# Kernel tuning notes

Measured on AMD Instinct MI355X. Metric: run time of the kernel, lower is better.

## Reference

```python
import jax, jax.numpy as jnp
import numpy as np

ALPHA = 1.5
A = 0.5
BANDWIDTH = 1.0
SPHERE_RADIUS = 1.0
HIDDEN = 1024
HEAD = 64
EPS_ACOS = 1e-07
EPS_NORM = 1e-12  # torch F.normalize clamp_min eps


def _l2norm(v):
    # F.normalize(v, p=2, dim=-1)
    n = jnp.sqrt(jnp.sum(v * v, axis=-1, keepdims=True))
    return v / jnp.maximum(n, EPS_NORM)


def setup_inputs() -> dict:
    key = jax.random.key(0)
    ks = jax.random.split(key, 7)
    B, S = 8, 2048
    s = 1.0 / np.sqrt(HIDDEN)
    return {
        "x": jax.random.normal(ks[0], (B, S, HIDDEN), dtype=jnp.float32),
        "Wq": jax.random.uniform(ks[1], (HIDDEN, HEAD), jnp.float32, -s, s),
        "bq": jax.random.uniform(ks[2], (HEAD,), jnp.float32, -s, s),
        "Wk": jax.random.uniform(ks[3], (HIDDEN, HEAD), jnp.float32, -s, s),
        "bk": jax.random.uniform(ks[4], (HEAD,), jnp.float32, -s, s),
        "Wv": jax.random.uniform(ks[5], (HIDDEN, HEAD), jnp.float32, -s, s),
        "bv": jax.random.uniform(ks[6], (HEAD,), jnp.float32, -s, s),
    }


def reference(x, Wq, bq, Wk, bk, Wv, bv):
    # q,k,v: [B,S,HEAD], L2-normalized along feature axis
    q = _l2norm(jnp.einsum("bsh,hd->bsd", x, Wq) + bq)
    k = _l2norm(jnp.einsum("bsh,hd->bsd", x, Wk) + bk)
    v = _l2norm(jnp.einsum("bsh,hd->bsd", x, Wv) + bv)

    # geodesic distance on sphere: [B,S,S]
    cos = jnp.einsum("bqd,bkd->bqk", q, k)
    g_dist = jnp.arccos(jnp.clip(cos, -1.0 + EPS_ACOS, 1.0 - EPS_ACOS)) * SPHERE_RADIUS

    # alpha < 2 -> power-law score
    score = (1.0 + g_dist / jnp.sqrt(BANDWIDTH)) ** (-HEAD - ALPHA)

    # dual degree normalization (a != 0): diag(row^-a) @ S @ diag(col^-a),
    # expressed as broadcast row/col scaling (same math, no diag_embed matmuls)
    r = jnp.sum(score, axis=-1) ** (-A)  # [B,Sq]
    c = jnp.sum(score, axis=-2) ** (-A)  # [B,Sk]
    k_tilde = r[..., :, None] * score * c[..., None, :]

    # L1 normalize over key axis (F.normalize p=1): entries are positive
    denom = jnp.maximum(jnp.sum(jnp.abs(k_tilde), axis=-1, keepdims=True), EPS_NORM)
    probs = k_tilde / denom

    out = jnp.einsum("bqk,bkd->bqd", probs, v)
    return (out, probs)
```

## Files before the change

kernel.cpp:

```cpp
#include <hip/hip_runtime.h>
#include <math.h>

#define BB 8
#define SS 2048
#define HH 1024
#define DD 64
#define NCV 65

typedef __attribute__((ext_vector_type(8))) short bf16x8;
typedef __attribute__((ext_vector_type(4))) float f32x4;
typedef __attribute__((ext_vector_type(16))) float f32x16;

#define MFMA16(a, b, c) __builtin_amdgcn_mfma_f32_16x16x32_bf16(a, b, c, 0, 0, 0)
#define MFMA32(a, b, c) __builtin_amdgcn_mfma_f32_32x32x16_bf16(a, b, c, 0, 0, 0)

__device__ __forceinline__ ushort bf16rne(float f) {
    uint u = __float_as_uint(f);
    uint r = (u + 0x7FFFu + ((u >> 16) & 1u)) >> 16;
    return (ushort)r;
}
__device__ __forceinline__ float bf2f(ushort h) {
    return __uint_as_float(((uint)h) << 16);
}

__device__ __forceinline__ float score_fn(float cosv) {
    float ax = fminf(fabsf(cosv), 1.0f - 1e-7f);
    float p = fmaf(ax, -0.0012624911f, 0.0066700901f);
    p = fmaf(ax, p, -0.0170881256f);
    p = fmaf(ax, p, 0.0308918810f);
    p = fmaf(ax, p, -0.0501743046f);
    p = fmaf(ax, p, 0.0889789874f);
    p = fmaf(ax, p, -0.2145988016f);
    p = fmaf(ax, p, 1.5707963050f);
    float r = sqrtf(1.0f - ax) * p;
    float g = (cosv >= 0.0f) ? r : (3.14159265358979f - r);
    return exp2f(-65.5f * log2f(1.0f + g));
}

__global__ __launch_bounds__(256) void k_prep(
    const float* __restrict__ Wq, const float* __restrict__ Wk, const float* __restrict__ Wv,
    const float* __restrict__ bq, const float* __restrict__ bk, const float* __restrict__ bv,
    ushort* __restrict__ Whi, ushort* __restrict__ Wlo, float* __restrict__ bcat)
{
    const int n = blockIdx.x;
    const int m = n >> 6, d = n & 63;
    const float* W = (m == 0) ? Wq : (m == 1 ? Wk : Wv);
    #pragma unroll
    for (int i = 0; i < 4; ++i) {
        int j = i * 256 + threadIdx.x;
        float f = W[(size_t)j * DD + d];
        ushort h = bf16rne(f);
        Whi[(size_t)n * HH + j] = h;
        Wlo[(size_t)n * HH + j] = bf16rne(f - bf2f(h));
    }
    if (n == 0 && threadIdx.x < 192) {
        int t = threadIdx.x, mm = t >> 6, dd = t & 63;
        const float* b = (mm == 0) ? bq : (mm == 1 ? bk : bv);
        bcat[t] = b[dd];
    }
}

__global__ __launch_bounds__(256) void k_projmm(
    const float* __restrict__ x, const ushort* __restrict__ Whi,
    const ushort* __restrict__ Wlo, const float* __restrict__ bcat,
    ushort* __restrict__ qh, ushort* __restrict__ ql,
    ushort* __restrict__ kh, ushort* __restrict__ kl,
    float* __restrict__ vw)
{
    __shared__ __align__(16) char smem[32 * 193 * 4];
    __shared__ float rns[96];
    __shared__ float bsh[192];
    ushort* xhi = (ushort*)smem;
    ushort* xlo = xhi + 32 * 128;
    float* ctile = (float*)smem;

    const int t = threadIdx.x;
    const int lane = t & 63;
    const int wid = t >> 6;
    const int row0 = blockIdx.x * 32;
    if (t < 192) bsh[t] = bcat[t];

    f32x4 acc[2][3];
    #pragma unroll
    for (int ar = 0; ar < 2; ++ar)
        #pragma unroll
        for (int bc = 0; bc < 3; ++bc)
            acc[ar][bc] = (f32x4){0.f, 0.f, 0.f, 0.f};

    for (int ch = 0; ch < 8; ++ch) {
        const int j0 = ch * 128;
        __syncthreads();
        #pragma unroll
        for (int i = 0; i < 2; ++i) {
            int u = i * 256 + t;
            int row = u >> 4, uc = u & 15;
            const float* xp = &x[(size_t)(row0 + row) * HH + j0 + uc * 8];
            float4 a = *(const float4*)xp;
            float4 b = *(const float4*)(xp + 4);
            float fs[8] = {a.x, a.y, a.z, a.w, b.x, b.y, b.z, b.w};
            bf16x8 hv, lv;
            #pragma unroll
            for (int e = 0; e < 8; ++e) {
                ushort h = bf16rne(fs[e]);
                hv[e] = (short)h;
                lv[e] = (short)bf16rne(fs[e] - bf2f(h));
            }
            int su = uc ^ (row & 7);
            *(bf16x8*)(xhi + row * 128 + su * 8) = hv;
            *(bf16x8*)(xlo + row * 128 + su * 8) = lv;
        }
        __syncthreads();
        #pragma unroll
        for (int ks = 0; ks < 4; ++ks) {
            bf16x8 ah[2], al[2], bh[3], bl[3];
            #pragma unroll
            for (int ar = 0; ar < 2; ++ar) {
                int row = ar * 16 + (lane & 15);
                int su = (ks * 4 + (lane >> 4)) ^ (row & 7);
                ah[ar] = *(const bf16x8*)(xhi + row * 128 + su * 8);
                al[ar] = *(const bf16x8*)(xlo + row * 128 + su * 8);
            }
            const int koff = j0 + ks * 32 + (lane >> 4) * 8;
            #pragma unroll
            for (int bc = 0; bc < 3; ++bc) {
                int n = wid * 48 + bc * 16 + (lane & 15);
                bh[bc] = *(const bf16x8*)(Whi + (size_t)n * HH + koff);
                bl[bc] = *(const bf16x8*)(Wlo + (size_t)n * HH + koff);
            }
            #pragma unroll
            for (int ar = 0; ar < 2; ++ar)
                #pragma unroll
                for (int bc = 0; bc < 3; ++bc) {
                    acc[ar][bc] = MFMA16(ah[ar], bh[bc], acc[ar][bc]);
                    acc[ar][bc] = MFMA16(ah[ar], bl[bc], acc[ar][bc]);
                    acc[ar][bc] = MFMA16(al[ar], bh[bc], acc[ar][bc]);
                }
        }
    }
    __syncthreads();
    #pragma unroll
    for (int ar = 0; ar < 2; ++ar)
        #pragma unroll
        for (int bc = 0; bc < 3; ++bc) {
            int n = wid * 48 + bc * 16 + (lane & 15);
            #pragma unroll
            for (int r = 0; r < 4; ++r) {
                int row = ar * 16 + (lane >> 4) * 4 + r;
                ctile[row * 193 + n] = acc[ar][bc][r];
            }
        }
    __syncthreads();
    if (t < 96) {
        int mat = t >> 5, row = t & 31;
        float ss = 0.f;
        #pragma unroll 8
        for (int d = 0; d < 64; ++d) {
            float v = ctile[row * 193 + mat * 64 + d] + bsh[mat * 64 + d];
            ss = fmaf(v, v, ss);
        }
        rns[t] = 1.0f / fmaxf(sqrtf(ss), 1e-12f);
    }
    __syncthreads();
    #pragma unroll
    for (int i = 0; i < 24; ++i) {
        int idx = i * 256 + t;
        int row = idx / 192;
        int n = idx - row * 192;
        float v = (ctile[row * 193 + n] + bsh[n]) * rns[(n >> 6) * 32 + row];
        size_t off = (size_t)(row0 + row) * DD + (n & 63);
        if (n < 64) {
            ushort h = bf16rne(v);
            qh[off] = h; ql[off] = bf16rne(v - bf2f(h));
        } else if (n < 128) {
            ushort h = bf16rne(v);
            kh[off] = h; kl[off] = bf16rne(v - bf2f(h));
        } else {
            vw[off] = v;
        }
    }
}

#define K_LOAD(H0,H1,H2,H3,L0,L1,L2,L3, KT) { \
    const ushort* kp = kh + (size_t)(b * SS + kbase + (KT) * 32 + qrow) * DD + kg; \
    const ushort* lp = kl + (size_t)(b * SS + kbase + (KT) * 32 + qrow) * DD + kg; \
    H0 = *(const bf16x8*)(kp);      L0 = *(const bf16x8*)(lp); \
    H1 = *(const bf16x8*)(kp + 16); L1 = *(const bf16x8*)(lp + 16); \
    H2 = *(const bf16x8*)(kp + 32); L2 = *(const bf16x8*)(lp + 32); \
    H3 = *(const bf16x8*)(kp + 48); L3 = *(const bf16x8*)(lp + 48); }

#define K_COMPUTE(H0,H1,H2,H3,L0,L1,L2,L3, KT) { \
    f32x16 acc = Z16; \
    acc = MFMA32(H0, qbh0, acc); acc = MFMA32(H0, qbl0, acc); acc = MFMA32(L0, qbh0, acc); \
    acc = MFMA32(H1, qbh1, acc); acc = MFMA32(H1, qbl1, acc); acc = MFMA32(L1, qbh1, acc); \
    acc = MFMA32(H2, qbh2, acc); acc = MFMA32(H2, qbl2, acc); acc = MFMA32(L2, qbh2, acc); \
    acc = MFMA32(H3, qbh3, acc); acc = MFMA32(H3, qbl3, acc); acc = MFMA32(L3, qbh3, acc); \
    const int kloc = kbase + (KT) * 32 + hi4; \
    uint2 wv; \
    wv.x = (uint)bf16rne(score_fn(acc[0]))  | ((uint)bf16rne(score_fn(acc[1]))  << 16); \
    wv.y = (uint)bf16rne(score_fn(acc[2]))  | ((uint)bf16rne(score_fn(acc[3]))  << 16); \
    *(uint2*)(srow + kloc) = wv; \
    wv.x = (uint)bf16rne(score_fn(acc[4]))  | ((uint)bf16rne(score_fn(acc[5]))  << 16); \
    wv.y = (uint)bf16rne(score_fn(acc[6]))  | ((uint)bf16rne(score_fn(acc[7]))  << 16); \
    *(uint2*)(srow + kloc + 8) = wv; \
    wv.x = (uint)bf16rne(score_fn(acc[8]))  | ((uint)bf16rne(score_fn(acc[9]))  << 16); \
    wv.y = (uint)bf16rne(score_fn(acc[10])) | ((uint)bf16rne(score_fn(acc[11])) << 16); \
    *(uint2*)(srow + kloc + 16) = wv; \
    wv.x = (uint)bf16rne(score_fn(acc[12])) | ((uint)bf16rne(score_fn(acc[13])) << 16); \
    wv.y = (uint)bf16rne(score_fn(acc[14])) | ((uint)bf16rne(score_fn(acc[15])) << 16); \
    *(uint2*)(srow + kloc + 24) = wv; }

__global__ __launch_bounds__(256, 4) void k_score(
    const ushort* __restrict__ qh, const ushort* __restrict__ ql,
    const ushort* __restrict__ kh, const ushort* __restrict__ kl,
    ushort* __restrict__ scrS)
{
    const int t = threadIdx.x;
    const int lane = t & 63;
    const int w = t >> 6;
    const int bid = blockIdx.x;
    const int b  = bid >> 8;
    const int q0 = ((bid >> 2) & 63) * 32;
    const int kbase = (bid & 3) * 512 + w * 128;
    const int qrow = lane & 31;
    const int kg = (lane >> 5) * 8;
    const int hi4 = (lane >> 5) * 4;
    const f32x16 Z16 = {0.f,0.f,0.f,0.f,0.f,0.f,0.f,0.f,0.f,0.f,0.f,0.f,0.f,0.f,0.f,0.f};

    const size_t qoff = (size_t)(b * SS + q0 + qrow) * DD + kg;
    bf16x8 qbh0 = *(const bf16x8*)(qh + qoff);
    bf16x8 qbh1 = *(const bf16x8*)(qh + qoff + 16);
    bf16x8 qbh2 = *(const bf16x8*)(qh + qoff + 32);
    bf16x8 qbh3 = *(const bf16x8*)(qh + qoff + 48);
    bf16x8 qbl0 = *(const bf16x8*)(ql + qoff);
    bf16x8 qbl1 = *(const bf16x8*)(ql + qoff + 16);
    bf16x8 qbl2 = *(const bf16x8*)(ql + qoff + 32);
    bf16x8 qbl3 = *(const bf16x8*)(ql + qoff + 48);
    ushort* srow = scrS + (size_t)(b * SS + q0 + qrow) * 4096 + 2048;

    bf16x8 xh0, xh1, xh2, xh3, xl0, xl1, xl2, xl3;
    bf16x8 yh0, yh1, yh2, yh3, yl0, yl1, yl2, yl3;
    K_LOAD(xh0,xh1,xh2,xh3,xl0,xl1,xl2,xl3, 0)
    K_LOAD(yh0,yh1,yh2,yh3,yl0,yl1,yl2,yl3, 1)
    K_COMPUTE(xh0,xh1,xh2,xh3,xl0,xl1,xl2,xl3, 0)
    K_LOAD(xh0,xh1,xh2,xh3,xl0,xl1,xl2,xl3, 2)
    K_COMPUTE(yh0,yh1,yh2,yh3,yl0,yl1,yl2,yl3, 1)
    K_LOAD(yh0,yh1,yh2,yh3,yl0,yl1,yl2,yl3, 3)
    K_COMPUTE(xh0,xh1,xh2,xh3,xl0,xl1,xl2,xl3, 2)
    K_COMPUTE(yh0,yh1,yh2,yh3,yl0,yl1,yl2,yl3, 3)
}

__global__ __launch_bounds__(256) void k_csum(
    const ushort* __restrict__ scrS, float* __restrict__ colsum)
{
    __shared__ float cls[32][64];
    const int t = threadIdx.x;
    const int bid = blockIdx.x;
    const int b  = bid >> 8;
    const int k0 = ((bid >> 3) & 31) * 64;
    const int qs = (bid & 7) * 256;
    const int tq = t >> 3, tk = t & 7;
    float colacc[8];
    #pragma unroll
    for (int e = 0; e < 8; ++e) colacc[e] = 0.f;
    #pragma unroll 2
    for (int it = 0; it < 8; ++it) {
        int q = qs + it * 32 + tq;
        bf16x8 s8 = *(const bf16x8*)(scrS + (size_t)(b * SS + q) * 4096 + 2048 + k0 + tk * 8);
        #pragma unroll
        for (int e = 0; e < 8; ++e) colacc[e] += bf2f((ushort)s8[e]);
    }
    #pragma unroll
    for (int e = 0; e < 8; ++e) cls[tq][tk * 8 + e] = colacc[e];
    __syncthreads();
    if (t < 64) {
        float s = 0.f;
        #pragma unroll
        for (int i = 0; i < 32; ++i) s += cls[i][t];
        atomicAdd(&colsum[b * SS + k0 + t], s);
    }
}

__global__ __launch_bounds__(256) void k_cvc(
    const float* __restrict__ vw, const float* __restrict__ colsum,
    ushort* __restrict__ cvT)
{
    __shared__ float vs[128][68];
    const int t = threadIdx.x;
    const int b = blockIdx.x >> 4;
    const int k0 = (blockIdx.x & 15) * 128;
    #pragma unroll
    for (int i = 0; i < 8; ++i) {
        int idx = i * 256 + t;
        int r = idx >> 4, c4 = idx & 15;
        float4 v4 = *(const float4*)&vw[(size_t)(b * SS + k0 + r) * DD + c4 * 4];
        *(float4*)&vs[r][c4 * 4] = v4;
    }
    __syncthreads();
    const int tk = t & 127;
    const int tj = t >> 7;
    float c = 1.0f / sqrtf(colsum[b * SS + k0 + tk]);
    #pragma unroll
    for (int jj = 0; jj < 32; ++jj) {
        int j = jj * 2 + tj;
        cvT[((size_t)b * NCV + j) * SS + k0 + tk] = bf16rne(c * vs[tk][j]);
    }
    if (tj == 0) cvT[((size_t)b * NCV + 64) * SS + k0 + tk] = bf16rne(c);
}

__global__ __launch_bounds__(256, 4) void k_nd(
    const ushort* __restrict__ scrS, const ushort* __restrict__ cvT,
    float* __restrict__ dinv_g, float* __restrict__ out)
{
    __shared__ float nred[16][64];
    __shared__ float dPart[4][16];
    __shared__ float dInv[16];
    const int t = threadIdx.x;
    const int lane = t & 63;
    const int w = t >> 6;
    const int b = blockIdx.x >> 7;
    const int q0 = (blockIdx.x & 127) * 16;
    const int kbase = w * 512;
    const int qn = lane & 15;
    const int g = lane >> 4;

    ((float*)nred)[t] = 0.f; ((float*)nred)[t + 256] = 0.f;
    ((float*)nred)[t + 512] = 0.f; ((float*)nred)[t + 768] = 0.f;
    __syncthreads();

    const ushort* cslice = cvT + (size_t)b * NCV * SS;
    const ushort* cbrow = cslice + (size_t)64 * SS;
    const ushort* srow = scrS + (size_t)(b * SS + q0 + qn) * 4096 + 2048;

    float dacc = 0.f;
    f32x4 nacc[4];
    #pragma unroll
    for (int ct = 0; ct < 4; ++ct) nacc[ct] = (f32x4){0.f, 0.f, 0.f, 0.f};

    #pragma unroll 4
    for (int ch = 0; ch < 16; ++ch) {
        const int ks0 = kbase + ch * 32;
        bf16x8 s8 = *(const bf16x8*)(srow + ks0 + g * 8);
        bf16x8 c8 = *(const bf16x8*)(cbrow + ks0 + g * 8);
        #pragma unroll
        for (int e = 0; e < 8; ++e)
            dacc = fmaf(bf2f((ushort)s8[e]), bf2f((ushort)c8[e]), dacc);
        #pragma unroll
        for (int ct = 0; ct < 4; ++ct) {
            bf16x8 bfv = *(const bf16x8*)(cslice + (size_t)(ct * 16 + qn) * SS + ks0 + g * 8);
            nacc[ct] = MFMA16(s8, bfv, nacc[ct]);
        }
    }
    {
        float d = dacc;
        d += __shfl_xor(d, 16, 64);
        d += __shfl_xor(d, 32, 64);
        if (lane < 16) dPart[w][lane] = d;
    }
    __syncthreads();
    if (t < 16) {
        float di = 1.0f / (dPart[0][t] + dPart[1][t] + dPart[2][t] + dPart[3][t]);
        dInv[t] = di;
        dinv_g[b * SS + q0 + t] = di;
    }
    #pragma unroll
    for (int ct = 0; ct < 4; ++ct)
        #pragma unroll
        for (int r = 0; r < 4; ++r)
            atomicAdd(&nred[g * 4 + r][ct * 16 + qn], nacc[ct][r]);
    __syncthreads();
    {
        int q = t >> 4, c4 = (t & 15) * 4;
        float di = dInv[q];
        float4 o;
        o.x = nred[q][c4] * di;     o.y = nred[q][c4 + 1] * di;
        o.z = nred[q][c4 + 2] * di; o.w = nred[q][c4 + 3] * di;
        *(float4*)&out[(size_t)(b * SS + q0 + q) * DD + c4] = o;
    }
}

__global__ __launch_bounds__(256) void k_probs(
    const ushort* __restrict__ scrS, const ushort* __restrict__ cvT,
    const float* __restrict__ dinv_g, float* __restrict__ probs)
{
    const int t = threadIdx.x;
    const int b = blockIdx.x >> 8;
    const int r0 = (blockIdx.x & 255) * 8;
    const ushort* cbrow = cvT + ((size_t)b * NCV + 64) * SS;

    float cf[8];
    {
        bf16x8 c8 = *(const bf16x8*)(cbrow + t * 8);
        #pragma unroll
        for (int e = 0; e < 8; ++e) cf[e] = bf2f((ushort)c8[e]);
    }
    bf16x8 s8[8];
    float di[8];
    #pragma unroll
    for (int r = 0; r < 8; ++r) {
        s8[r] = *(const bf16x8*)(scrS + (size_t)(b * SS + r0 + r) * 4096 + 2048 + t * 8);
        di[r] = dinv_g[b * SS + r0 + r];
    }
    __syncthreads();
    #pragma unroll
    for (int r = 0; r < 8; ++r) {
        float4 o0, o1;
        o0.x = bf2f((ushort)s8[r][0]) * cf[0] * di[r];
        o0.y = bf2f((ushort)s8[r][1]) * cf[1] * di[r];
        o0.z = bf2f((ushort)s8[r][2]) * cf[2] * di[r];
        o0.w = bf2f((ushort)s8[r][3]) * cf[3] * di[r];
        o1.x = bf2f((ushort)s8[r][4]) * cf[4] * di[r];
        o1.y = bf2f((ushort)s8[r][5]) * cf[5] * di[r];
        o1.z = bf2f((ushort)s8[r][6]) * cf[6] * di[r];
        o1.w = bf2f((ushort)s8[r][7]) * cf[7] * di[r];
        float* prow = probs + (size_t)(b * SS + r0 + r) * SS + t * 8;
        *(float4*)prow = o0;
        *(float4*)(prow + 4) = o1;
    }
}

extern "C" void kernel_launch(void* const* d_in, const int* in_sizes, int n_in,
                              void* d_out, int out_size, void* d_ws, size_t ws_size,
                              hipStream_t stream)
{
    const float* x  = (const float*)d_in[0];
    const float* Wq = (const float*)d_in[1];
    const float* bq = (const float*)d_in[2];
    const float* Wk = (const float*)d_in[3];
    const float* bk = (const float*)d_in[4];
    const float* Wv = (const float*)d_in[5];
    const float* bv = (const float*)d_in[6];

    float* out   = (float*)d_out;
    float* probs = out + (size_t)BB * SS * DD;
    ushort* scrS = (ushort*)probs;

    const size_t NQ = (size_t)BB * SS * DD;
    ushort* qh    = (ushort*)d_ws;
    ushort* ql    = qh + NQ;
    ushort* kh    = ql + NQ;
    ushort* kl    = kh + NQ;
    float*  vw    = (float*)(kl + NQ);
    float*  colsum = vw + NQ;
    float*  dinv  = colsum + BB * SS;
    ushort* cvT   = (ushort*)(dinv + BB * SS);
    ushort* Whi   = cvT + (size_t)BB * NCV * SS;
    ushort* Wlo   = Whi + (size_t)192 * HH;
    float*  bcat  = (float*)(Wlo + (size_t)192 * HH);

    hipMemsetAsync(colsum, 0, BB * SS * sizeof(float), stream);
    k_prep  <<<192, 256, 0, stream>>>(Wq, Wk, Wv, bq, bk, bv, Whi, Wlo, bcat);
    k_projmm<<<512, 256, 0, stream>>>(x, Whi, Wlo, bcat, qh, ql, kh, kl, vw);
    k_score <<<2048, 256, 0, stream>>>(qh, ql, kh, kl, scrS);
    k_csum  <<<2048, 256, 0, stream>>>(scrS, colsum);
    k_cvc   <<<128, 256, 0, stream>>>(vw, colsum, cvT);
    k_nd    <<<1024, 256, 0, stream>>>(scrS, cvT, dinv, out);
    k_probs <<<2048, 256, 0, stream>>>(scrS, cvT, dinv, probs);
}
```

Measured before the change: 227.4 us.

## Fuse normalization and probs write into one kernel; coalesce cvT writes

Merges the denominator/output kernel with the probs-writing kernel, so each block computes its row inverse degree in shared memory and then writes its own probs rows. This removes the global dinv buffer and one kernel launch, and the second read of the score rows is more likely to hit cache. The k_cvc transpose now works on 64-column tiles and writes packed 4-element chunks so stores are coalesced. Also switches to the library bf16 conversion, uses pointer-increment addressing in the MFMA loop, and writes probs with nontemporal stores. The in-place aliasing of scores inside the probs buffer stays correct only because each block reads its own rows before the barrier that precedes overwriting them.

```diff
diff --git a/kernel.cpp b/kernel.cpp
--- a/kernel.cpp
+++ b/kernel.cpp
@@ -1,4 +1,5 @@
 #include <hip/hip_runtime.h>
+#include <hip/hip_bf16.h>
 #include <math.h>
 
 #define BB 8
@@ -18,6 +19,10 @@
     uint u = __float_as_uint(f);
     uint r = (u + 0x7FFFu + ((u >> 16) & 1u)) >> 16;
     return (ushort)r;
+}
+__device__ __forceinline__ ushort bfc(float f) {
+    __hip_bfloat16 h = __float2bfloat16(f);
+    return *reinterpret_cast<ushort*>(&h);
 }
 __device__ __forceinline__ float bf2f(ushort h) {
     return __uint_as_float(((uint)h) << 16);
@@ -196,17 +201,17 @@
     acc = MFMA32(H3, qbh3, acc); acc = MFMA32(H3, qbl3, acc); acc = MFMA32(L3, qbh3, acc); \
     const int kloc = kbase + (KT) * 32 + hi4; \
     uint2 wv; \
-    wv.x = (uint)bf16rne(score_fn(acc[0]))  | ((uint)bf16rne(score_fn(acc[1]))  << 16); \
-    wv.y = (uint)bf16rne(score_fn(acc[2]))  | ((uint)bf16rne(score_fn(acc[3]))  << 16); \
+    wv.x = (uint)bfc(score_fn(acc[0]))  | ((uint)bfc(score_fn(acc[1]))  << 16); \
+    wv.y = (uint)bfc(score_fn(acc[2]))  | ((uint)bfc(score_fn(acc[3]))  << 16); \
     *(uint2*)(srow + kloc) = wv; \
-    wv.x = (uint)bf16rne(score_fn(acc[4]))  | ((uint)bf16rne(score_fn(acc[5]))  << 16); \
-    wv.y = (uint)bf16rne(score_fn(acc[6]))  | ((uint)bf16rne(score_fn(acc[7]))  << 16); \
+    wv.x = (uint)bfc(score_fn(acc[4]))  | ((uint)bfc(score_fn(acc[5]))  << 16); \
+    wv.y = (uint)bfc(score_fn(acc[6]))  | ((uint)bfc(score_fn(acc[7]))  << 16); \
     *(uint2*)(srow + kloc + 8) = wv; \
-    wv.x = (uint)bf16rne(score_fn(acc[8]))  | ((uint)bf16rne(score_fn(acc[9]))  << 16); \
-    wv.y = (uint)bf16rne(score_fn(acc[10])) | ((uint)bf16rne(score_fn(acc[11])) << 16); \
+    wv.x = (uint)bfc(score_fn(acc[8]))  | ((uint)bfc(score_fn(acc[9]))  << 16); \
+    wv.y = (uint)bfc(score_fn(acc[10])) | ((uint)bfc(score_fn(acc[11])) << 16); \
     *(uint2*)(srow + kloc + 16) = wv; \
-    wv.x = (uint)bf16rne(score_fn(acc[12])) | ((uint)bf16rne(score_fn(acc[13])) << 16); \
-    wv.y = (uint)bf16rne(score_fn(acc[14])) | ((uint)bf16rne(score_fn(acc[15])) << 16); \
+    wv.x = (uint)bfc(score_fn(acc[12])) | ((uint)bfc(score_fn(acc[13])) << 16); \
+    wv.y = (uint)bfc(score_fn(acc[14])) | ((uint)bfc(score_fn(acc[15])) << 16); \
     *(uint2*)(srow + kloc + 24) = wv; }
 
 __global__ __launch_bounds__(256, 4) void k_score(
@@ -284,32 +289,42 @@
     const float* __restrict__ vw, const float* __restrict__ colsum,
     ushort* __restrict__ cvT)
 {
-    __shared__ float vs[128][68];
+    __shared__ float vs[64][65];
+    __shared__ float csh[64];
     const int t = threadIdx.x;
-    const int b = blockIdx.x >> 4;
-    const int k0 = (blockIdx.x & 15) * 128;
-    #pragma unroll
-    for (int i = 0; i < 8; ++i) {
+    const int b = blockIdx.x >> 5;
+    const int k0 = (blockIdx.x & 31) * 64;
+    #pragma unroll
+    for (int i = 0; i < 4; ++i) {
         int idx = i * 256 + t;
         int r = idx >> 4, c4 = idx & 15;
         float4 v4 = *(const float4*)&vw[(size_t)(b * SS + k0 + r) * DD + c4 * 4];
         *(float4*)&vs[r][c4 * 4] = v4;
     }
-    __syncthreads();
-    const int tk = t & 127;
-    const int tj = t >> 7;
-    float c = 1.0f / sqrtf(colsum[b * SS + k0 + tk]);
-    #pragma unroll
-    for (int jj = 0; jj < 32; ++jj) {
-        int j = jj * 2 + tj;
-        cvT[((size_t)b * NCV + j) * SS + k0 + tk] = bf16rne(c * vs[tk][j]);
-    }
-    if (tj == 0) cvT[((size_t)b * NCV + 64) * SS + k0 + tk] = bf16rne(c);
-}
-
-__global__ __launch_bounds__(256, 4) void k_nd(
+    if (t < 64) csh[t] = 1.0f / sqrtf(colsum[b * SS + k0 + t]);
+    __syncthreads();
+    const int kk4 = (t & 15) * 4;
+    #pragma unroll
+    for (int jt = 0; jt < 4; ++jt) {
+        int j = jt * 16 + (t >> 4);
+        uint2 wv;
+        wv.x = (uint)bfc(csh[kk4 + 0] * vs[kk4 + 0][j])
+             | ((uint)bfc(csh[kk4 + 1] * vs[kk4 + 1][j]) << 16);
+        wv.y = (uint)bfc(csh[kk4 + 2] * vs[kk4 + 2][j])
+             | ((uint)bfc(csh[kk4 + 3] * vs[kk4 + 3][j]) << 16);
+        *(uint2*)(cvT + ((size_t)b * NCV + j) * SS + k0 + kk4) = wv;
+    }
+    if (t < 16) {
+        uint2 wv;
+        wv.x = (uint)bfc(csh[t * 4 + 0]) | ((uint)bfc(csh[t * 4 + 1]) << 16);
+        wv.y = (uint)bfc(csh[t * 4 + 2]) | ((uint)bfc(csh[t * 4 + 3]) << 16);
+        *(uint2*)(cvT + ((size_t)b * NCV + 64) * SS + k0 + t * 4) = wv;
+    }
+}
+
+__global__ __launch_bounds__(256, 4) void k_ndp(
     const ushort* __restrict__ scrS, const ushort* __restrict__ cvT,
-    float* __restrict__ dinv_g, float* __restrict__ out)
+    float* __restrict__ probs, float* __restrict__ out)
 {
     __shared__ float nred[16][64];
     __shared__ float dPart[4][16];
@@ -329,26 +344,35 @@
 
     const ushort* cslice = cvT + (size_t)b * NCV * SS;
     const ushort* cbrow = cslice + (size_t)64 * SS;
-    const ushort* srow = scrS + (size_t)(b * SS + q0 + qn) * 4096 + 2048;
 
     float dacc = 0.f;
     f32x4 nacc[4];
     #pragma unroll
     for (int ct = 0; ct < 4; ++ct) nacc[ct] = (f32x4){0.f, 0.f, 0.f, 0.f};
 
+    const ushort* sp = scrS + (size_t)(b * SS + q0 + qn) * 4096 + 2048 + kbase + g * 8;
+    const ushort* cp = cbrow + kbase + g * 8;
+    const ushort* p0 = cslice + (size_t)(0 * 16 + qn) * SS + kbase + g * 8;
+    const ushort* p1 = cslice + (size_t)(1 * 16 + qn) * SS + kbase + g * 8;
+    const ushort* p2 = cslice + (size_t)(2 * 16 + qn) * SS + kbase + g * 8;
+    const ushort* p3 = cslice + (size_t)(3 * 16 + qn) * SS + kbase + g * 8;
+
     #pragma unroll 4
     for (int ch = 0; ch < 16; ++ch) {
-        const int ks0 = kbase + ch * 32;
-        bf16x8 s8 = *(const bf16x8*)(srow + ks0 + g * 8);
-        bf16x8 c8 = *(const bf16x8*)(cbrow + ks0 + g * 8);
+        bf16x8 s8 = *(const bf16x8*)sp;
+        bf16x8 c8 = *(const bf16x8*)cp;
+        bf16x8 b0 = *(const bf16x8*)p0;
+        bf16x8 b1 = *(const bf16x8*)p1;
+        bf16x8 b2 = *(const bf16x8*)p2;
+        bf16x8 b3 = *(const bf16x8*)p3;
         #pragma unroll
         for (int e = 0; e < 8; ++e)
             dacc = fmaf(bf2f((ushort)s8[e]), bf2f((ushort)c8[e]), dacc);
-        #pragma unroll
-        for (int ct = 0; ct < 4; ++ct) {
-            bf16x8 bfv = *(const bf16x8*)(cslice + (size_t)(ct * 16 + qn) * SS + ks0 + g * 8);
-            nacc[ct] = MFMA16(s8, bfv, nacc[ct]);
-        }
+        nacc[0] = MFMA16(s8, b0, nacc[0]);
+        nacc[1] = MFMA16(s8, b1, nacc[1]);
+        nacc[2] = MFMA16(s8, b2, nacc[2]);
+        nacc[3] = MFMA16(s8, b3, nacc[3]);
+        sp += 32; cp += 32; p0 += 32; p1 += 32; p2 += 32; p3 += 32;
     }
     {
         float d = dacc;
@@ -357,11 +381,7 @@
         if (lane < 16) dPart[w][lane] = d;
     }
     __syncthreads();
-    if (t < 16) {
-        float di = 1.0f / (dPart[0][t] + dPart[1][t] + dPart[2][t] + dPart[3][t]);
-        dInv[t] = di;
-        dinv_g[b * SS + q0 + t] = di;
-    }
+    if (t < 16) dInv[t] = 1.0f / (dPart[0][t] + dPart[1][t] + dPart[2][t] + dPart[3][t]);
     #pragma unroll
     for (int ct = 0; ct < 4; ++ct)
         #pragma unroll
@@ -376,45 +396,38 @@
         o.z = nred[q][c4 + 2] * di; o.w = nred[q][c4 + 3] * di;
         *(float4*)&out[(size_t)(b * SS + q0 + q) * DD + c4] = o;
     }
-}
-
-__global__ __launch_bounds__(256) void k_probs(
-    const ushort* __restrict__ scrS, const ushort* __restrict__ cvT,
-    const float* __restrict__ dinv_g, float* __restrict__ probs)
-{
-    const int t = threadIdx.x;
-    const int b = blockIdx.x >> 8;
-    const int r0 = (blockIdx.x & 255) * 8;
-    const ushort* cbrow = cvT + ((size_t)b * NCV + 64) * SS;
-
     float cf[8];
     {
         bf16x8 c8 = *(const bf16x8*)(cbrow + t * 8);
         #pragma unroll
         for (int e = 0; e < 8; ++e) cf[e] = bf2f((ushort)c8[e]);
     }
-    bf16x8 s8[8];
-    float di[8];
-    #pragma unroll
-    for (int r = 0; r < 8; ++r) {
-        s8[r] = *(const bf16x8*)(scrS + (size_t)(b * SS + r0 + r) * 4096 + 2048 + t * 8);
-        di[r] = dinv_g[b * SS + r0 + r];
-    }
-    __syncthreads();
-    #pragma unroll
-    for (int r = 0; r < 8; ++r) {
-        float4 o0, o1;
-        o0.x = bf2f((ushort)s8[r][0]) * cf[0] * di[r];
-        o0.y = bf2f((ushort)s8[r][1]) * cf[1] * di[r];
-        o0.z = bf2f((ushort)s8[r][2]) * cf[2] * di[r];
-        o0.w = bf2f((ushort)s8[r][3]) * cf[3] * di[r];
-        o1.x = bf2f((ushort)s8[r][4]) * cf[4] * di[r];
-        o1.y = bf2f((ushort)s8[r][5]) * cf[5] * di[r];
-        o1.z = bf2f((ushort)s8[r][6]) * cf[6] * di[r];
-        o1.w = bf2f((ushort)s8[r][7]) * cf[7] * di[r];
-        float* prow = probs + (size_t)(b * SS + r0 + r) * SS + t * 8;
-        *(float4*)prow = o0;
-        *(float4*)(prow + 4) = o1;
+    #pragma unroll
+    for (int rb = 0; rb < 4; ++rb) {
+        bf16x8 s[4];
+        float dl[4];
+        #pragma unroll
+        for (int j = 0; j < 4; ++j) {
+            int row = rb * 4 + j;
+            s[j] = *(const bf16x8*)(scrS + (size_t)(b * SS + q0 + row) * 4096 + 2048 + t * 8);
+            dl[j] = dInv[row];
+        }
+        __syncthreads();
+        #pragma unroll
+        for (int j = 0; j < 4; ++j) {
+            f32x4 o0, o1;
+            o0[0] = bf2f((ushort)s[j][0]) * cf[0] * dl[j];
+            o0[1] = bf2f((ushort)s[j][1]) * cf[1] * dl[j];
+            o0[2] = bf2f((ushort)s[j][2]) * cf[2] * dl[j];
+            o0[3] = bf2f((ushort)s[j][3]) * cf[3] * dl[j];
+            o1[0] = bf2f((ushort)s[j][4]) * cf[4] * dl[j];
+            o1[1] = bf2f((ushort)s[j][5]) * cf[5] * dl[j];
+            o1[2] = bf2f((ushort)s[j][6]) * cf[6] * dl[j];
+            o1[3] = bf2f((ushort)s[j][7]) * cf[7] * dl[j];
+            float* prow = probs + (size_t)(b * SS + q0 + rb * 4 + j) * SS + t * 8;
+            __builtin_nontemporal_store(o0, (f32x4*)prow);
+            __builtin_nontemporal_store(o1, (f32x4*)(prow + 4));
+        }
     }
 }
 
@@ -441,8 +454,7 @@
     ushort* kl    = kh + NQ;
     float*  vw    = (float*)(kl + NQ);
     float*  colsum = vw + NQ;
-    float*  dinv  = colsum + BB * SS;
-    ushort* cvT   = (ushort*)(dinv + BB * SS);
+    ushort* cvT   = (ushort*)(colsum + BB * SS);
     ushort* Whi   = cvT + (size_t)BB * NCV * SS;
     ushort* Wlo   = Whi + (size_t)192 * HH;
     float*  bcat  = (float*)(Wlo + (size_t)192 * HH);
@@ -452,7 +464,6 @@
     k_projmm<<<512, 256, 0, stream>>>(x, Whi, Wlo, bcat, qh, ql, kh, kl, vw);
     k_score <<<2048, 256, 0, stream>>>(qh, ql, kh, kl, scrS);
     k_csum  <<<2048, 256, 0, stream>>>(scrS, colsum);
-    k_cvc   <<<128, 256, 0, stream>>>(vw, colsum, cvT);
-    k_nd    <<<1024, 256, 0, stream>>>(scrS, cvT, dinv, out);
-    k_probs <<<2048, 256, 0, stream>>>(scrS, cvT, dinv, probs);
-}
+    k_cvc   <<<256, 256, 0, stream>>>(vw, colsum, cvT);
+    k_ndp   <<<1024, 256, 0, stream>>>(scrS, cvT, probs, out);
+}
```

Result: no change. 224.6 us (-1.2%).
